# Performance work log

Measured on AMD Instinct MI355X. Metric: run time of the kernel, lower is better.

The kernel has to match this reference:

```python
import jax, jax.numpy as jnp
import numpy as np

D = 1024
H = 16
HD = D // H
EPS = 1e-9


def setup_inputs() -> dict:
    key = jax.random.key(0)
    ks = jax.random.split(key, 16)
    B, Lq, Lk = 8, 512, 1024
    s = 0.02
    return {
        "q": jax.random.normal(ks[0], (B, Lq, D), jnp.float32),
        "q_mask": jnp.ones((B, Lq), jnp.bool_),
        "kv": jax.random.normal(ks[1], (B, Lk, D), jnp.float32),
        "kv_mask": jnp.ones((B, Lk), jnp.bool_),
        # MultiheadAttention packed in-proj + out-proj
        "in_proj_w": jax.random.normal(ks[2], (3 * D, D), jnp.float32) * s,
        "in_proj_b": jnp.zeros((3 * D,), jnp.float32),
        "out_w": jax.random.normal(ks[3], (D, D), jnp.float32) * s,
        "out_b": jnp.zeros((D,), jnp.float32),
        # shared LayerNorm
        "ln_g": jnp.ones((D,), jnp.float32),
        "ln_b": jnp.zeros((D,), jnp.float32),
        # FFN
        "w1": jax.random.normal(ks[4], (4 * D, D), jnp.float32) * s,
        "b1": jnp.zeros((4 * D,), jnp.float32),
        "w2": jax.random.normal(ks[5], (D, 4 * D), jnp.float32) * s,
        "b2": jnp.zeros((D,), jnp.float32),
        # gate MLP
        "gw1": jax.random.normal(ks[6], (D, 2 * D), jnp.float32) * s,
        "gb1": jnp.zeros((D,), jnp.float32),
        "gw2": jax.random.normal(ks[7], (1, D), jnp.float32) * s,
        "gb2": jnp.zeros((1,), jnp.float32),
    }


def _layer_norm(x, g, b, eps=1e-5):
    mu = x.mean(-1, keepdims=True)
    var = ((x - mu) ** 2).mean(-1, keepdims=True)
    return (x - mu) * jax.lax.rsqrt(var + eps) * g + b


def reference(q, q_mask, kv, kv_mask, in_proj_w, in_proj_b, out_w, out_b,
              ln_g, ln_b, w1, b1, w2, b2, gw1, gb1, gw2, gb2):
    B, Lq, _ = q.shape
    Lk = kv.shape[1]
    # packed projections (torch Linear convention: x @ W.T + b)
    qp = (q @ in_proj_w[:D].T + in_proj_b[:D]).reshape(B, Lq, H, HD)
    kp = (kv @ in_proj_w[D:2 * D].T + in_proj_b[D:2 * D]).reshape(B, Lk, H, HD)
    vp = (kv @ in_proj_w[2 * D:].T + in_proj_b[2 * D:]).reshape(B, Lk, H, HD)
    scores = jnp.einsum('bqhd,bkhd->bhqk', qp, kp) / np.sqrt(HD)  # (B,H,Lq,Lk)
    scores = jnp.where(kv_mask[:, None, None, :], scores, -1e30)
    attn = jax.nn.softmax(scores, axis=-1)
    ctx = jnp.einsum('bhqk,bkhd->bqhd', attn, vp).reshape(B, Lq, D)
    attn_out = ctx @ out_w.T + out_b
    # entropy over keys, normalized by log(Lk), averaged over heads
    p = jnp.clip(attn, EPS)
    ent = -(p * jnp.log(p)).sum(-1) / jnp.log(jnp.float32(Lk))  # (B,H,Lq)
    ent = ent.mean(axis=1)[..., None]  # (B,Lq,1)
    conf = jnp.clip(1.0 - ent, 0.0, 1.0)
    # gate MLP on [q, attn_out]
    h = jax.nn.gelu(jnp.concatenate([q, attn_out], -1) @ gw1.T + gb1, approximate=False)
    g = jax.nn.sigmoid(h @ gw2.T + gb2) * conf
    q2 = _layer_norm(q + attn_out * g, ln_g, ln_b)
    ffn = jax.nn.gelu(q2 @ w1.T + b1, approximate=False) @ w2.T + b2
    q2 = _layer_norm(q2 + ffn, ln_g, ln_b)
    return q2, ent
```

## Files before the change

kernel.cpp:

```cpp
#include <hip/hip_runtime.h>
#include <cstdint>
#include <cstddef>

typedef __bf16 bf16;
typedef __bf16 bf16x8 __attribute__((ext_vector_type(8)));
typedef __bf16 bf16x4 __attribute__((ext_vector_type(4)));
typedef float  f32x4  __attribute__((ext_vector_type(4)));

#define GLOAD_LDS16(g, l) __builtin_amdgcn_global_load_lds( \
    (const __attribute__((address_space(1))) unsigned int*)(g), \
    (__attribute__((address_space(3))) unsigned int*)(l), 16, 0, 0)

static constexpr int D_  = 1024;
static constexpr int H_  = 16;
static constexpr int HD_ = 64;
static constexpr int B_  = 8;
static constexpr int LQ_ = 512;
static constexpr int LK_ = 1024;
static constexpr int MQ_ = B_ * LQ_;
static constexpr int MK_ = B_ * LK_;
static constexpr float LOG2E_ = 1.4426950408889634f;
static constexpr float INV_LN_LK_ = 0.14426950408889634f;
static constexpr float CSHIFT_ = 8.0f;

__device__ __forceinline__ float gelu_f(float v) {
    float v2 = v * v;
    float u = fmaf(0.035677408136f, v2, 0.7978845608028654f);
    float s = exp2f(v * u * -2.8853900817779268f);
    return v / (1.0f + s);
}

__global__ __launch_bounds__(256)
void cast_all_k(const float* __restrict__ ipw, const float* __restrict__ outw,
                const float* __restrict__ w1,  const float* __restrict__ w2,
                const float* __restrict__ gw1, const float* __restrict__ q,
                const float* __restrict__ kv,
                bf16* __restrict__ ipw_b, bf16* __restrict__ outw_b,
                bf16* __restrict__ w1_b,  bf16* __restrict__ w2_b,
                bf16* __restrict__ gw1_b, bf16* __restrict__ x_b,
                bf16* __restrict__ kv_b) {
    const int b = blockIdx.x, t = threadIdx.x;
    const float* src; bf16* dst; long e;
    if (b < 1536)       { src = ipw;  dst = ipw_b;  e = (long)b * 2048; }
    else if (b < 2048)  { src = outw; dst = outw_b; e = (long)(b - 1536) * 2048; }
    else if (b < 4096)  { src = w1;   dst = w1_b;   e = (long)(b - 2048) * 2048; }
    else if (b < 6144)  { src = w2;   dst = w2_b;   e = (long)(b - 4096) * 2048; }
    else if (b < 7168)  { src = gw1;  dst = gw1_b;  e = (long)(b - 6144) * 2048; }
    else if (b < 11264) { src = kv;   dst = kv_b;   e = (long)(b - 7168) * 2048; }
    else {
        long e2 = (long)(b - 11264) * 2048 + t * 8;
        float4 a = *(const float4*)(q + e2);
        float4 c = *(const float4*)(q + e2 + 4);
        bf16x8 o;
        o[0]=(bf16)a.x; o[1]=(bf16)a.y; o[2]=(bf16)a.z; o[3]=(bf16)a.w;
        o[4]=(bf16)c.x; o[5]=(bf16)c.y; o[6]=(bf16)c.z; o[7]=(bf16)c.w;
        long row = e2 >> 10, col = e2 & 1023;
        *(bf16x8*)(x_b + row * 2048 + col) = o;
        return;
    }
    e += t * 8;
    float4 a = *(const float4*)(src + e);
    float4 c = *(const float4*)(src + e + 4);
    bf16x8 o;
    o[0]=(bf16)a.x; o[1]=(bf16)a.y; o[2]=(bf16)a.z; o[3]=(bf16)a.w;
    o[4]=(bf16)c.x; o[5]=(bf16)c.y; o[6]=(bf16)c.z; o[7]=(bf16)c.w;
    *(bf16x8*)(dst + e) = o;
}

template<int SPLITK>
__device__ __forceinline__
void gemmP_body(const bf16* __restrict__ A, int lda,
                const bf16* __restrict__ W, int ldw,
                const float* __restrict__ bias,
                bf16* __restrict__ Cb0, bf16* __restrict__ Cb1, int ldcb,
                int K, int aoff, int woff) {
    __shared__ __attribute__((aligned(16))) bf16 LDSp[3 * 8192];
    const int gx = gridDim.x, gy = gridDim.y;
    const int nwg = gx * gy * gridDim.z;
    const int flat = blockIdx.x + gx * (blockIdx.y + gy * blockIdx.z);
    const int swz = (flat & 7) * (nwg >> 3) + (flat >> 3);
    int rem = swz, z = 0;
    if (SPLITK) { z = swz / (gx * gy); rem = swz - z * (gx * gy); }
    const int by = rem / gx, bx = rem - by * gx;
    if (SPLITK) { A += (size_t)z * aoff; W += (size_t)z * woff; }
    bf16* Cb = (SPLITK && z) ? Cb1 : Cb0;

    const int t = threadIdx.x;
    const int w = t >> 6, l = t & 63, l15 = l & 15, lg = l >> 4;
    const int row0 = by * 128, col0 = bx * 128;
    const int wr = (w >> 1) * 64, wc = (w & 1) * 64;

    const int sr = t >> 2;
    const int sc = ((t & 3) ^ ((sr >> 1) & 3)) << 3;
    const bf16* pA0 = A + (size_t)(row0 + sr) * lda + sc;
    const bf16* pA1 = A + (size_t)(row0 + 64 + sr) * lda + sc;
    const bf16* pW0 = W + (size_t)(col0 + sr) * ldw + sc;
    const bf16* pW1 = W + (size_t)(col0 + 64 + sr) * ldw + sc;
    const int lo0 = w * 512, lo1 = 2048 + w * 512;

    auto STAGE = [&](int kt, int slot) {
        bf16* base = (bf16*)LDSp + slot * 8192;
        const int kc = kt * 32;
        GLOAD_LDS16(pA0 + kc, base + lo0);
        GLOAD_LDS16(pA1 + kc, base + lo1);
        GLOAD_LDS16(pW0 + kc, base + 4096 + lo0);
        GLOAD_LDS16(pW1 + kc, base + 4096 + lo1);
    };

    f32x4 acc[4][4];
#pragma unroll
    for (int m = 0; m < 4; ++m)
#pragma unroll
        for (int n = 0; n < 4; ++n) acc[m][n] = f32x4{0.f, 0.f, 0.f, 0.f};

    const int nk = K >> 5;
    STAGE(0, 0); STAGE(1, 1);
    asm volatile("s_waitcnt vmcnt(4)" ::: "memory");
    __builtin_amdgcn_s_barrier();

    int s0 = 0, s1 = 1, s2 = 2;
    const int kcol = (lg ^ ((l15 >> 1) & 3)) << 3;
    for (int kt = 0; kt < nk; ++kt) {
        const bf16* bufA = (const bf16*)LDSp + s0 * 8192;
        const bf16* bufB = bufA + 4096;
        bf16x8 af[4], bf4[4];
#pragma unroll
        for (int m = 0; m < 4; ++m)
            af[m] = *(const bf16x8*)&bufA[(wr + m * 16 + l15) * 32 + kcol];
#pragma unroll
        for (int n = 0; n < 4; ++n)
            bf4[n] = *(const bf16x8*)&bufB[(wc + n * 16 + l15) * 32 + kcol];
        if (kt + 2 < nk) STAGE(kt + 2, s2);
        __builtin_amdgcn_s_setprio(1);
#pragma unroll
        for (int m = 0; m < 4; ++m)
#pragma unroll
            for (int n = 0; n < 4; ++n)
                acc[m][n] = __builtin_amdgcn_mfma_f32_16x16x32_bf16(af[m], bf4[n], acc[m][n], 0, 0, 0);
        __builtin_amdgcn_s_setprio(0);
        asm volatile("s_waitcnt lgkmcnt(0)" ::: "memory");
        __builtin_amdgcn_sched_barrier(0);
        if (kt + 2 < nk) {
            asm volatile("s_waitcnt vmcnt(4)" ::: "memory");
        } else {
            asm volatile("s_waitcnt vmcnt(0)" ::: "memory");
        }
        __builtin_amdgcn_s_barrier();
        const int tmp = s0; s0 = s1; s1 = s2; s2 = tmp;
    }

    float bvn[4];
#pragma unroll
    for (int n = 0; n < 4; ++n) bvn[n] = bias ? bias[col0 + wc + n * 16 + l15] : 0.f;
    const int erow = l >> 2, ec = (l & 3) * 16;
#pragma unroll
    for (int m = 0; m < 4; ++m) {
        bf16* ep = (bf16*)LDSp + ((m & 1) * 4 + w) * 1152;
#pragma unroll
        for (int n = 0; n < 4; ++n)
#pragma unroll
            for (int r = 0; r < 4; ++r)
                ep[(lg * 4 + r) * 72 + n * 16 + l15] = (bf16)(acc[m][n][r] + bvn[n]);
        asm volatile("s_waitcnt lgkmcnt(0)" ::: "memory");
        __builtin_amdgcn_sched_barrier(0);
        bf16x8 v8a = *(const bf16x8*)&ep[erow * 72 + ec];
        bf16x8 v8b = *(const bf16x8*)&ep[erow * 72 + ec + 8];
        const int grow = row0 + wr + m * 16 + erow;
        bf16* dst = Cb + (size_t)grow * ldcb + col0 + wc + ec;
        *(bf16x8*)dst = v8a;
        *(bf16x8*)(dst + 8) = v8b;
    }
}

__global__ __launch_bounds__(256, 2)
void gemmP_outproj_k(const bf16* A, const bf16* W, const float* bias, bf16* Cb) {
    gemmP_body<0>(A, 1024, W, 1024, bias, Cb, nullptr, 2048, 1024, 0, 0);
}
__global__ __launch_bounds__(256, 2)
void gemmP_gate2_k(const bf16* A, const bf16* W, bf16* C0, bf16* C1) {
    gemmP_body<1>(A, 2048, W, 2048, nullptr, C0, C1, 1024, 1024, 1024, 1024);
}
__global__ __launch_bounds__(256, 2)
void gemmP_ffn2_k(const bf16* A, const bf16* W, bf16* C0, bf16* C1) {
    gemmP_body<1>(A, 4096, W, 4096, nullptr, C0, C1, 1024, 2048, 2048, 2048);
}

template<int ACT, int ROWBIAS>
__device__ __forceinline__
void gemm128x256_body(bf16* LDSb, int by, int bx,
                      const bf16* __restrict__ A, int lda,
                      const bf16* __restrict__ W, int ldw,
                      const float* __restrict__ bias,
                      bf16* __restrict__ Cb, int ldcb, int K) {
    const int t = threadIdx.x;
    const int w = t >> 6, l = t & 63, l15 = l & 15, lg = l >> 4;
    const int wrr = w >> 2, wc = w & 3;
    const int row0 = by * 128, col0 = bx * 256;

    const int trow = t >> 2;
    const int scol = ((t & 3) ^ ((trow >> 1) & 3)) << 3;
    const bf16* pA  = A + (size_t)(row0 + trow) * lda + scol;
    const bf16* pB0 = W + (size_t)(col0 + trow) * ldw + scol;
    const bf16* pB1 = W + (size_t)(col0 + 128 + trow) * ldw + scol;
    const int ldsoA  = w * 512;
    const int ldsoB0 = 4096 + w * 512;
    const int ldsoB1 = 8192 + w * 512;

    f32x4 acc[4][4];
#pragma unroll
    for (int m = 0; m < 4; ++m)
#pragma unroll
        for (int n = 0; n < 4; ++n) acc[m][n] = f32x4{0.f, 0.f, 0.f, 0.f};

    const int nk = K >> 5;
    GLOAD_LDS16(pA,  LDSb + ldsoA);
    GLOAD_LDS16(pB0, LDSb + ldsoB0);
    GLOAD_LDS16(pB1, LDSb + ldsoB1);

    for (int kt = 0; kt < nk; ++kt) {
        const int cur = kt & 1;
        if (kt + 1 < nk) {
            const int kc = (kt + 1) * 32;
            bf16* d = LDSb + (cur ^ 1) * 12288;
            GLOAD_LDS16(pA + kc,  d + ldsoA);
            GLOAD_LDS16(pB0 + kc, d + ldsoB0);
            GLOAD_LDS16(pB1 + kc, d + ldsoB1);
            asm volatile("s_waitcnt vmcnt(3)" ::: "memory");
        } else {
            asm volatile("s_waitcnt vmcnt(0)" ::: "memory");
        }
        __builtin_amdgcn_s_barrier();
        const bf16* bufA = LDSb + cur * 12288;
        const bf16* bufB = bufA + 4096;
        const int kcol = (lg ^ ((l15 >> 1) & 3)) << 3;
        bf16x8 bf4[4];
#pragma unroll
        for (int n = 0; n < 4; ++n)
            bf4[n] = *(const bf16x8*)&bufB[(wc * 64 + n * 16 + l15) * 32 + kcol];
#pragma unroll
        for (int m = 0; m < 4; ++m) {
            bf16x8 afm = *(const bf16x8*)&bufA[(wrr * 64 + m * 16 + l15) * 32 + kcol];
#pragma unroll
            for (int n = 0; n < 4; ++n)
                acc[m][n] = __builtin_amdgcn_mfma_f32_16x16x32_bf16(afm, bf4[n], acc[m][n], 0, 0, 0);
        }
        asm volatile("s_waitcnt lgkmcnt(0)" ::: "memory");
        __builtin_amdgcn_sched_barrier(0);
        __builtin_amdgcn_s_barrier();
    }

    const int erow = l >> 2, ec = (l & 3) * 16;
    float bvn[4];
    if (!ROWBIAS) {
#pragma unroll
        for (int n = 0; n < 4; ++n) bvn[n] = bias[col0 + wc * 64 + n * 16 + l15];
    }
#pragma unroll
    for (int m = 0; m < 4; ++m) {
        float bvr[4];
        if (ROWBIAS) {
#pragma unroll
            for (int r = 0; r < 4; ++r)
                bvr[r] = bias[row0 + wrr * 64 + m * 16 + lg * 4 + r];
        }
        bf16* ep = LDSb + ((m & 1) * 8 + w) * 1152;
#pragma unroll
        for (int n = 0; n < 4; ++n)
#pragma unroll
            for (int r = 0; r < 4; ++r) {
                float v = acc[m][n][r] + (ROWBIAS ? bvr[r] : bvn[n]);
                if (ACT) v = gelu_f(v);
                ep[(lg * 4 + r) * 72 + n * 16 + l15] = (bf16)v;
            }
        asm volatile("s_waitcnt lgkmcnt(0)" ::: "memory");
        __builtin_amdgcn_sched_barrier(0);
        bf16x8 v8a = *(const bf16x8*)&ep[erow * 72 + ec];
        bf16x8 v8b = *(const bf16x8*)&ep[erow * 72 + ec + 8];
        const int grow = row0 + wrr * 64 + m * 16 + erow;
        bf16* dst = Cb + (size_t)grow * ldcb + col0 + wc * 64 + ec;
        *(bf16x8*)dst = v8a;
        *(bf16x8*)(dst + 8) = v8b;
    }
}

__global__ __launch_bounds__(512, 4)
void gemm_proj3_k(const bf16* __restrict__ xb, const bf16* __restrict__ kvb,
                  const bf16* __restrict__ ipw_b, const float* __restrict__ ipb,
                  bf16* __restrict__ Qp, bf16* __restrict__ Kp, bf16* __restrict__ Vt) {
    __shared__ __attribute__((aligned(16))) bf16 LDSb[2 * 12288];
    const int fb = blockIdx.x;
    if (fb < 256) {
        const int id = fb;
        const int swz = (id & 7) * 32 + (id >> 3);
        gemm128x256_body<0, 0>(LDSb, swz >> 2, swz & 3, kvb, 1024, ipw_b + 1024 * 1024, 1024,
                               ipb + 1024, Kp, 1024, 1024);
    } else if (fb < 512) {
        const int id = fb - 256;
        const int bx = (id & 7) * 4 + ((id >> 3) & 3);
        const int by = id >> 5;
        gemm128x256_body<0, 1>(LDSb, by, bx, ipw_b + 2048 * 1024, 1024, kvb, 1024,
                               ipb + 2048, Vt, 8192, 1024);
    } else {
        const int id = fb - 512;
        const int swz = (id & 7) * 16 + (id >> 3);
        gemm128x256_body<0, 0>(LDSb, swz >> 2, swz & 3, xb, 2048, ipw_b, 1024, ipb, Qp, 1024, 1024);
    }
}

__global__ __launch_bounds__(512, 4)
void gemmA_ffn1_k(const bf16* A, const bf16* W, const float* bias, bf16* Cb) {
    __shared__ __attribute__((aligned(16))) bf16 LDSb[2 * 12288];
    const int f = blockIdx.x + gridDim.x * blockIdx.y;
    const int x = f & 7, i = f >> 3;
    const int by = (x >> 1) * 8 + (i >> 3);
    const int bx = (x & 1) * 8 + (i & 7);
    gemm128x256_body<1, 0>(LDSb, by, bx, A, 1024, W, 1024, bias, Cb, 4096, 1024);
}

__device__ __forceinline__ float red16sum(float v) {
    v += __shfl_xor(v, 1, 64);
    v += __shfl_xor(v, 2, 64);
    v += __shfl_xor(v, 4, 64);
    v += __shfl_xor(v, 8, 64);
    return v;
}

__global__ __launch_bounds__(256)
void attn_k(const bf16* __restrict__ Qp, const bf16* __restrict__ Kp,
            const bf16* __restrict__ Vt, bf16* __restrict__ ctx,
            float* __restrict__ entm) {
    __shared__ __attribute__((aligned(16))) bf16 Ks[64 * 64];
    __shared__ __attribute__((aligned(16))) bf16 Vs[64 * 64];
    __shared__ __attribute__((aligned(16))) bf16 Ps[4][16 * 72];
    const int t = threadIdx.x, w = t >> 6, l = t & 63;
    const int l15 = l & 15, lg = l >> 4;
    const int h = blockIdx.x, b = blockIdx.y, qt = blockIdx.z;
    const int qrow0 = b * LQ_ + qt * 64 + w * 16;

    bf16x8 aq[2];
#pragma unroll
    for (int kk = 0; kk < 2; ++kk)
        aq[kk] = *(const bf16x8*)(Qp + (size_t)(qrow0 + l15) * D_ + h * HD_ + kk * 32 + lg * 8);

    const int r0 = t >> 3, r1 = 32 + (t >> 3), j = t & 7;
    const bf16* pK0 = Kp + (size_t)(b * LK_ + r0) * 1024 + h * HD_ + ((j ^ (r0 & 7)) << 3);
    const bf16* pK1 = Kp + (size_t)(b * LK_ + r1) * 1024 + h * HD_ + ((j ^ (r1 & 7)) << 3);
    const bf16* pV0 = Vt + (size_t)(h * HD_ + r0) * (size_t)MK_ + b * LK_ + ((j ^ (r0 & 7)) << 3);
    const bf16* pV1 = Vt + (size_t)(h * HD_ + r1) * (size_t)MK_ + b * LK_ + ((j ^ (r1 & 7)) << 3);
    const int ldsoL = w * 512, ldsoH = 2048 + w * 512;

    auto STAGE = [&](int c) {
        const size_t kadv = (size_t)c * 64 * 1024;
        const size_t vadv = (size_t)c * 64;
        GLOAD_LDS16(pK0 + kadv, (bf16*)Ks + ldsoL);
        GLOAD_LDS16(pK1 + kadv, (bf16*)Ks + ldsoH);
        GLOAD_LDS16(pV0 + vadv, (bf16*)Vs + ldsoL);
        GLOAD_LDS16(pV1 + vadv, (bf16*)Vs + ldsoH);
    };

    f32x4 o[4];
    float Zp[4], S1p[4];
#pragma unroll
    for (int n = 0; n < 4; ++n) o[n] = f32x4{0.f, 0.f, 0.f, 0.f};
#pragma unroll
    for (int r = 0; r < 4; ++r) { Zp[r] = 0.f; S1p[r] = 0.f; }

    const float K1 = 0.125f * LOG2E_;
    const float K0 = -CSHIFT_ * LOG2E_;
    const int swk = l15 & 7;

    for (int c = 0; c < LK_ / 64; ++c) {
        STAGE(c);
        asm volatile("s_waitcnt vmcnt(0)" ::: "memory");
        __builtin_amdgcn_s_barrier();

        f32x4 s[4];
#pragma unroll
        for (int n = 0; n < 4; ++n) {
            s[n] = f32x4{0.f, 0.f, 0.f, 0.f};
#pragma unroll
            for (int kk = 0; kk < 2; ++kk) {
                bf16x8 bk = *(const bf16x8*)&Ks[(n * 16 + l15) * 64 + ((((kk << 2) | lg) ^ swk) << 3)];
                s[n] = __builtin_amdgcn_mfma_f32_16x16x32_bf16(aq[kk], bk, s[n], 0, 0, 0);
            }
        }

        float p[4][4];
#pragma unroll
        for (int r = 0; r < 4; ++r) {
#pragma unroll
            for (int n = 0; n < 4; ++n) {
                float sv = s[n][r];
                float pv = exp2f(fmaf(sv, K1, K0));
                p[n][r] = pv;
                Zp[r] += pv;
                S1p[r] = fmaf(pv, sv, S1p[r]);
            }
        }

#pragma unroll
        for (int r = 0; r < 4; ++r)
#pragma unroll
            for (int n = 0; n < 4; ++n)
                Ps[w][(lg * 4 + r) * 72 + ((n ^ lg) << 4) + l15] = (bf16)p[n][r];

        bf16x8 ap[2];
#pragma unroll
        for (int kk = 0; kk < 2; ++kk)
            ap[kk] = *(const bf16x8*)&Ps[w][l15 * 72 + ((kk * 32 + lg * 8) ^ (((l15 >> 2) & 3) << 4))];
#pragma unroll
        for (int n = 0; n < 4; ++n)
#pragma unroll
            for (int kk = 0; kk < 2; ++kk) {
                bf16x8 bv = *(const bf16x8*)&Vs[(n * 16 + l15) * 64 + ((((kk << 2) | lg) ^ swk) << 3)];
                o[n] = __builtin_amdgcn_mfma_f32_16x16x32_bf16(ap[kk], bv, o[n], 0, 0, 0);
            }

        asm volatile("s_waitcnt lgkmcnt(0)" ::: "memory");
        __builtin_amdgcn_sched_barrier(0);
        __builtin_amdgcn_s_barrier();
    }

#pragma unroll
    for (int r = 0; r < 4; ++r) {
        float Zr = red16sum(Zp[r]);
        float S1r = red16sum(S1p[r]) * 0.125f;
        float inv = 1.0f / Zr;
        int grow = qrow0 + lg * 4 + r;
#pragma unroll
        for (int n = 0; n < 4; ++n)
            ctx[(size_t)grow * D_ + h * HD_ + n * 16 + l15] = (bf16)(o[n][r] * inv);
        if (l15 == 0) {
            float ent = (CSHIFT_ + logf(Zr) - S1r * inv) * INV_LN_LK_ * (1.0f / 16.0f);
            atomicAdd(&entm[grow], ent);
        }
    }
}

__device__ __forceinline__ float blk_sum(float v, float* sb) {
#pragma unroll
    for (int m = 1; m < 64; m <<= 1) v += __shfl_xor(v, m, 64);
    int w = threadIdx.x >> 6;
    __syncthreads();
    if ((threadIdx.x & 63) == 0) sb[w] = v;
    __syncthreads();
    return sb[0] + sb[1] + sb[2] + sb[3];
}
__device__ __forceinline__ float2 blk_sum2(float2 v, float* sb) {
#pragma unroll
    for (int m = 1; m < 64; m <<= 1) {
        v.x += __shfl_xor(v.x, m, 64);
        v.y += __shfl_xor(v.y, m, 64);
    }
    int w = threadIdx.x >> 6;
    __syncthreads();
    if ((threadIdx.x & 63) == 0) { sb[w * 2] = v.x; sb[w * 2 + 1] = v.y; }
    __syncthreads();
    return make_float2(sb[0] + sb[2] + sb[4] + sb[6], sb[1] + sb[3] + sb[5] + sb[7]);
}

__global__ __launch_bounds__(256)
void gate_ln1_k(const float* __restrict__ qin, const bf16* __restrict__ xb,
                const bf16* __restrict__ gp0, const bf16* __restrict__ gp1,
                const float* __restrict__ gb1, const float* __restrict__ gw2,
                const float* __restrict__ gb2, const float* __restrict__ entm,
                const float* __restrict__ lng, const float* __restrict__ lnb,
                bf16* __restrict__ q2b) {
    __shared__ float sb[8];
    const int row = blockIdx.x, t = threadIdx.x, c0 = t * 4;
    bf16x4 pa = *(const bf16x4*)(gp0 + (size_t)row * D_ + c0);
    bf16x4 pb = *(const bf16x4*)(gp1 + (size_t)row * D_ + c0);
    float4 hb = *(const float4*)(gb1 + c0);
    float h0 = gelu_f((float)pa[0] + (float)pb[0] + hb.x);
    float h1 = gelu_f((float)pa[1] + (float)pb[1] + hb.y);
    float h2 = gelu_f((float)pa[2] + (float)pb[2] + hb.z);
    float h3 = gelu_f((float)pa[3] + (float)pb[3] + hb.w);
    float4 g4 = *(const float4*)(gw2 + c0);
    float dot = h0 * g4.x + h1 * g4.y + h2 * g4.z + h3 * g4.w;
    dot = blk_sum(dot, sb);
    float g = 1.0f / (1.0f + expf(-(dot + gb2[0])));
    float conf = fminf(fmaxf(1.0f - entm[row], 0.0f), 1.0f);
    g *= conf;
    float4 qv = *(const float4*)(qin + (size_t)row * D_ + c0);
    bf16x4 a4 = *(const bf16x4*)(xb + (size_t)row * 2048 + 1024 + c0);
    float y[4] = { qv.x + (float)a4[0] * g, qv.y + (float)a4[1] * g,
                   qv.z + (float)a4[2] * g, qv.w + (float)a4[3] * g };
    float2 ss = blk_sum2(make_float2(y[0] + y[1] + y[2] + y[3],
                                     y[0]*y[0] + y[1]*y[1] + y[2]*y[2] + y[3]*y[3]), sb);
    float mu = ss.x * (1.0f / D_);
    float var = ss.y * (1.0f / D_) - mu * mu;
    float rs = rsqrtf(var + 1e-5f);
    float4 gg = *(const float4*)(lng + c0);
    float4 bb = *(const float4*)(lnb + c0);
    bf16x4 ob;
    ob[0] = (bf16)((y[0] - mu) * rs * gg.x + bb.x);
    ob[1] = (bf16)((y[1] - mu) * rs * gg.y + bb.y);
    ob[2] = (bf16)((y[2] - mu) * rs * gg.z + bb.z);
    ob[3] = (bf16)((y[3] - mu) * rs * gg.w + bb.w);
    *(bf16x4*)(q2b + (size_t)row * D_ + c0) = ob;
}

__global__ __launch_bounds__(256)
void ln2_k(const bf16* __restrict__ q2b, const bf16* __restrict__ fp0,
           const bf16* __restrict__ fp1, const float* __restrict__ b2,
           const float* __restrict__ lng, const float* __restrict__ lnb,
           float* __restrict__ outp) {
    __shared__ float sb[8];
    const int row = blockIdx.x, t = threadIdx.x, c0 = t * 4;
    bf16x4 a4 = *(const bf16x4*)(q2b + (size_t)row * D_ + c0);
    bf16x4 f0 = *(const bf16x4*)(fp0 + (size_t)row * D_ + c0);
    bf16x4 f1 = *(const bf16x4*)(fp1 + (size_t)row * D_ + c0);
    float4 bv = *(const float4*)(b2 + c0);
    float y[4] = { (float)a4[0] + (float)f0[0] + (float)f1[0] + bv.x,
                   (float)a4[1] + (float)f0[1] + (float)f1[1] + bv.y,
                   (float)a4[2] + (float)f0[2] + (float)f1[2] + bv.z,
                   (float)a4[3] + (float)f0[3] + (float)f1[3] + bv.w };
    float2 ss = blk_sum2(make_float2(y[0] + y[1] + y[2] + y[3],
                                     y[0]*y[0] + y[1]*y[1] + y[2]*y[2] + y[3]*y[3]), sb);
    float mu = ss.x * (1.0f / D_);
    float var = ss.y * (1.0f / D_) - mu * mu;
    float rs = rsqrtf(var + 1e-5f);
    float4 gg = *(const float4*)(lng + c0);
    float4 bb = *(const float4*)(lnb + c0);
    *(float4*)(outp + (size_t)row * D_ + c0) = make_float4(
        (y[0] - mu) * rs * gg.x + bb.x, (y[1] - mu) * rs * gg.y + bb.y,
        (y[2] - mu) * rs * gg.z + bb.z, (y[3] - mu) * rs * gg.w + bb.w);
}

extern "C" void kernel_launch(void* const* d_in, const int* in_sizes, int n_in,
                              void* d_out, int out_size, void* d_ws, size_t ws_size,
                              hipStream_t stream) {
    (void)in_sizes; (void)n_in; (void)out_size; (void)ws_size;
    const float* q    = (const float*)d_in[0];
    const float* kv   = (const float*)d_in[2];
    const float* ipw  = (const float*)d_in[4];
    const float* ipb  = (const float*)d_in[5];
    const float* outw = (const float*)d_in[6];
    const float* outb = (const float*)d_in[7];
    const float* lng  = (const float*)d_in[8];
    const float* lnb  = (const float*)d_in[9];
    const float* w1   = (const float*)d_in[10];
    const float* b1   = (const float*)d_in[11];
    const float* w2   = (const float*)d_in[12];
    const float* b2   = (const float*)d_in[13];
    const float* gw1  = (const float*)d_in[14];
    const float* gb1  = (const float*)d_in[15];
    const float* gw2  = (const float*)d_in[16];
    const float* gb2  = (const float*)d_in[17];

    char* ws = (char*)d_ws;
    const size_t MB = 1u << 20;
    bf16*  ipw_b  = (bf16*)(ws + 0);
    bf16*  outw_b = (bf16*)(ws + 6 * MB);
    bf16*  w1_b   = (bf16*)(ws + 8 * MB);
    bf16*  w2_b   = (bf16*)(ws + 16 * MB);
    bf16*  gw1_b  = (bf16*)(ws + 24 * MB);
    bf16*  x_b    = (bf16*)(ws + 28 * MB);
    bf16*  kv_b   = (bf16*)(ws + 44 * MB);
    bf16*  Qp     = (bf16*)(ws + 60 * MB);
    bf16*  Kp     = (bf16*)(ws + 68 * MB);
    bf16*  Vt     = (bf16*)(ws + 84 * MB);
    bf16*  ctx    = (bf16*)(ws + 100 * MB);
    bf16*  gp0    = (bf16*)(ws + 44 * MB);
    bf16*  gp1    = (bf16*)(ws + 52 * MB);
    bf16*  q2b    = (bf16*)(ws + 100 * MB);
    bf16*  h1     = (bf16*)(ws + 44 * MB);
    bf16*  fp0    = (bf16*)(ws + 28 * MB);
    bf16*  fp1    = (bf16*)(ws + 0);

    float* out  = (float*)d_out;
    float* entm = out + (size_t)MQ_ * D_;

    (void)hipMemsetAsync(entm, 0, (size_t)MQ_ * sizeof(float), stream);

    cast_all_k<<<13312, 256, 0, stream>>>(ipw, outw, w1, w2, gw1, q, kv,
                                          ipw_b, outw_b, w1_b, w2_b, gw1_b, x_b, kv_b);

    gemm_proj3_k<<<640, 512, 0, stream>>>(x_b, kv_b, ipw_b, ipb, Qp, Kp, Vt);
    attn_k<<<dim3(H_, B_, LQ_ / 64), 256, 0, stream>>>(Qp, Kp, Vt, ctx, entm);
    gemmP_outproj_k<<<dim3(8, 32), 256, 0, stream>>>(ctx, outw_b, outb, x_b + 1024);
    gemmP_gate2_k<<<dim3(8, 32, 2), 256, 0, stream>>>(x_b, gw1_b, gp0, gp1);
    gate_ln1_k<<<MQ_, 256, 0, stream>>>(q, x_b, gp0, gp1, gb1, gw2, gb2, entm, lng, lnb, q2b);
    gemmA_ffn1_k<<<dim3(16, 32), 512, 0, stream>>>(q2b, w1_b, b1, h1);
    gemmP_ffn2_k<<<dim3(8, 32, 2), 256, 0, stream>>>(h1, w2_b, fp0, fp1);
    ln2_k<<<MQ_, 256, 0, stream>>>(q2b, fp0, fp1, b2, lng, lnb, out);
}
```

Measured before the change: 276.9 us.

## Restructure split-K GEMMs, merge out-proj with gate half, widen attention blocks

```diff
diff --git a/kernel.cpp b/kernel.cpp
--- a/kernel.cpp
+++ b/kernel.cpp
@@ -67,24 +67,12 @@
     *(bf16x8*)(dst + e) = o;
 }
 
-template<int SPLITK>
 __device__ __forceinline__
-void gemmP_body(const bf16* __restrict__ A, int lda,
+void gemmP_core(bf16* LDSp, int by, int bx,
+                const bf16* __restrict__ A, int lda,
                 const bf16* __restrict__ W, int ldw,
                 const float* __restrict__ bias,
-                bf16* __restrict__ Cb0, bf16* __restrict__ Cb1, int ldcb,
-                int K, int aoff, int woff) {
-    __shared__ __attribute__((aligned(16))) bf16 LDSp[3 * 8192];
-    const int gx = gridDim.x, gy = gridDim.y;
-    const int nwg = gx * gy * gridDim.z;
-    const int flat = blockIdx.x + gx * (blockIdx.y + gy * blockIdx.z);
-    const int swz = (flat & 7) * (nwg >> 3) + (flat >> 3);
-    int rem = swz, z = 0;
-    if (SPLITK) { z = swz / (gx * gy); rem = swz - z * (gx * gy); }
-    const int by = rem / gx, bx = rem - by * gx;
-    if (SPLITK) { A += (size_t)z * aoff; W += (size_t)z * woff; }
-    bf16* Cb = (SPLITK && z) ? Cb1 : Cb0;
-
+                bf16* __restrict__ Cb, int ldcb, int K) {
     const int t = threadIdx.x;
     const int w = t >> 6, l = t & 63, l15 = l & 15, lg = l >> 4;
     const int row0 = by * 128, col0 = bx * 128;
@@ -99,7 +87,7 @@
     const int lo0 = w * 512, lo1 = 2048 + w * 512;
 
     auto STAGE = [&](int kt, int slot) {
-        bf16* base = (bf16*)LDSp + slot * 8192;
+        bf16* base = LDSp + slot * 8192;
         const int kc = kt * 32;
         GLOAD_LDS16(pA0 + kc, base + lo0);
         GLOAD_LDS16(pA1 + kc, base + lo1);
@@ -121,7 +109,7 @@
     int s0 = 0, s1 = 1, s2 = 2;
     const int kcol = (lg ^ ((l15 >> 1) & 3)) << 3;
     for (int kt = 0; kt < nk; ++kt) {
-        const bf16* bufA = (const bf16*)LDSp + s0 * 8192;
+        const bf16* bufA = LDSp + s0 * 8192;
         const bf16* bufB = bufA + 4096;
         bf16x8 af[4], bf4[4];
 #pragma unroll
@@ -155,7 +143,7 @@
     const int erow = l >> 2, ec = (l & 3) * 16;
 #pragma unroll
     for (int m = 0; m < 4; ++m) {
-        bf16* ep = (bf16*)LDSp + ((m & 1) * 4 + w) * 1152;
+        bf16* ep = LDSp + ((m & 1) * 4 + w) * 1152;
 #pragma unroll
         for (int n = 0; n < 4; ++n)
 #pragma unroll
@@ -173,16 +161,42 @@
 }
 
 __global__ __launch_bounds__(256, 2)
-void gemmP_outproj_k(const bf16* A, const bf16* W, const float* bias, bf16* Cb) {
-    gemmP_body<0>(A, 1024, W, 1024, bias, Cb, nullptr, 2048, 1024, 0, 0);
-}
+void gemm_opq_k(const bf16* __restrict__ ctx, const bf16* __restrict__ outw_b,
+                const float* __restrict__ outb, const bf16* __restrict__ xb,
+                const bf16* __restrict__ gw1_b, bf16* __restrict__ ao_out,
+                bf16* __restrict__ gp0) {
+    __shared__ __attribute__((aligned(16))) bf16 LDSp[3 * 8192];
+    const int fb = blockIdx.x;
+    const int id = fb & 255;
+    const int swz = (id & 7) * 32 + (id >> 3);
+    const int by = swz >> 3, bx = swz & 7;
+    if (fb < 256)
+        gemmP_core(LDSp, by, bx, ctx, 1024, outw_b, 1024, outb, ao_out, 2048, 1024);
+    else
+        gemmP_core(LDSp, by, bx, xb, 2048, gw1_b, 2048, nullptr, gp0, 1024, 1024);
+}
+
 __global__ __launch_bounds__(256, 2)
-void gemmP_gate2_k(const bf16* A, const bf16* W, bf16* C0, bf16* C1) {
-    gemmP_body<1>(A, 2048, W, 2048, nullptr, C0, C1, 1024, 1024, 1024, 1024);
-}
+void gemm_gatek_k(const bf16* __restrict__ xb, const bf16* __restrict__ gw1_b,
+                  bf16* __restrict__ gp1) {
+    __shared__ __attribute__((aligned(16))) bf16 LDSp[3 * 8192];
+    const int id = blockIdx.x;
+    const int swz = (id & 7) * 32 + (id >> 3);
+    gemmP_core(LDSp, swz >> 3, swz & 7, xb + 1024, 2048, gw1_b + 1024, 2048,
+               nullptr, gp1, 1024, 1024);
+}
+
 __global__ __launch_bounds__(256, 2)
-void gemmP_ffn2_k(const bf16* A, const bf16* W, bf16* C0, bf16* C1) {
-    gemmP_body<1>(A, 4096, W, 4096, nullptr, C0, C1, 1024, 2048, 2048, 2048);
+void gemm_ffn2_k(const bf16* __restrict__ h1, const bf16* __restrict__ w2_b,
+                 bf16* __restrict__ f0, bf16* __restrict__ f1,
+                 bf16* __restrict__ f2, bf16* __restrict__ f3) {
+    __shared__ __attribute__((aligned(16))) bf16 LDSp[3 * 8192];
+    const int flat = blockIdx.x;
+    const int swz = (flat & 7) * 128 + (flat >> 3);
+    const int z = swz >> 8, rem = swz & 255;
+    bf16* Cb = (z == 0) ? f0 : (z == 1) ? f1 : (z == 2) ? f2 : f3;
+    gemmP_core(LDSp, rem >> 3, rem & 7, h1 + z * 1024, 4096, w2_b + z * 1024, 4096,
+               nullptr, Cb, 1024, 1024);
 }
 
 template<int ACT, int ROWBIAS>
@@ -325,37 +339,31 @@
     return v;
 }
 
-__global__ __launch_bounds__(256)
+__global__ __launch_bounds__(512)
 void attn_k(const bf16* __restrict__ Qp, const bf16* __restrict__ Kp,
             const bf16* __restrict__ Vt, bf16* __restrict__ ctx,
             float* __restrict__ entm) {
     __shared__ __attribute__((aligned(16))) bf16 Ks[64 * 64];
     __shared__ __attribute__((aligned(16))) bf16 Vs[64 * 64];
-    __shared__ __attribute__((aligned(16))) bf16 Ps[4][16 * 72];
+    __shared__ __attribute__((aligned(16))) bf16 Ps[8][16 * 72];
     const int t = threadIdx.x, w = t >> 6, l = t & 63;
     const int l15 = l & 15, lg = l >> 4;
     const int h = blockIdx.x, b = blockIdx.y, qt = blockIdx.z;
-    const int qrow0 = b * LQ_ + qt * 64 + w * 16;
+    const int qrow0 = b * LQ_ + qt * 128 + w * 16;
 
     bf16x8 aq[2];
 #pragma unroll
     for (int kk = 0; kk < 2; ++kk)
         aq[kk] = *(const bf16x8*)(Qp + (size_t)(qrow0 + l15) * D_ + h * HD_ + kk * 32 + lg * 8);
 
-    const int r0 = t >> 3, r1 = 32 + (t >> 3), j = t & 7;
-    const bf16* pK0 = Kp + (size_t)(b * LK_ + r0) * 1024 + h * HD_ + ((j ^ (r0 & 7)) << 3);
-    const bf16* pK1 = Kp + (size_t)(b * LK_ + r1) * 1024 + h * HD_ + ((j ^ (r1 & 7)) << 3);
-    const bf16* pV0 = Vt + (size_t)(h * HD_ + r0) * (size_t)MK_ + b * LK_ + ((j ^ (r0 & 7)) << 3);
-    const bf16* pV1 = Vt + (size_t)(h * HD_ + r1) * (size_t)MK_ + b * LK_ + ((j ^ (r1 & 7)) << 3);
-    const int ldsoL = w * 512, ldsoH = 2048 + w * 512;
+    const int r = t >> 3, j = t & 7;
+    const bf16* pK = Kp + (size_t)(b * LK_ + r) * 1024 + h * HD_ + ((j ^ (r & 7)) << 3);
+    const bf16* pV = Vt + (size_t)(h * HD_ + r) * (size_t)MK_ + b * LK_ + ((j ^ (r & 7)) << 3);
+    const int ldso = w * 512;
 
     auto STAGE = [&](int c) {
-        const size_t kadv = (size_t)c * 64 * 1024;
-        const size_t vadv = (size_t)c * 64;
-        GLOAD_LDS16(pK0 + kadv, (bf16*)Ks + ldsoL);
-        GLOAD_LDS16(pK1 + kadv, (bf16*)Ks + ldsoH);
-        GLOAD_LDS16(pV0 + vadv, (bf16*)Vs + ldsoL);
-        GLOAD_LDS16(pV1 + vadv, (bf16*)Vs + ldsoH);
+        GLOAD_LDS16(pK + (size_t)c * 64 * 1024, (bf16*)Ks + ldso);
+        GLOAD_LDS16(pV + (size_t)c * 64,        (bf16*)Vs + ldso);
     };
 
     f32x4 o[4];
@@ -363,7 +371,7 @@
 #pragma unroll
     for (int n = 0; n < 4; ++n) o[n] = f32x4{0.f, 0.f, 0.f, 0.f};
 #pragma unroll
-    for (int r = 0; r < 4; ++r) { Zp[r] = 0.f; S1p[r] = 0.f; }
+    for (int r2 = 0; r2 < 4; ++r2) { Zp[r2] = 0.f; S1p[r2] = 0.f; }
 
     const float K1 = 0.125f * LOG2E_;
     const float K0 = -CSHIFT_ * LOG2E_;
@@ -387,22 +395,22 @@
 
         float p[4][4];
 #pragma unroll
-        for (int r = 0; r < 4; ++r) {
+        for (int r2 = 0; r2 < 4; ++r2) {
 #pragma unroll
             for (int n = 0; n < 4; ++n) {
-                float sv = s[n][r];
+                float sv = s[n][r2];
                 float pv = exp2f(fmaf(sv, K1, K0));
-                p[n][r] = pv;
-                Zp[r] += pv;
-                S1p[r] = fmaf(pv, sv, S1p[r]);
+                p[n][r2] = pv;
+                Zp[r2] += pv;
+                S1p[r2] = fmaf(pv, sv, S1p[r2]);
             }
         }
 
 #pragma unroll
-        for (int r = 0; r < 4; ++r)
+        for (int r2 = 0; r2 < 4; ++r2)
 #pragma unroll
             for (int n = 0; n < 4; ++n)
-                Ps[w][(lg * 4 + r) * 72 + ((n ^ lg) << 4) + l15] = (bf16)p[n][r];
+                Ps[w][(lg * 4 + r2) * 72 + ((n ^ lg) << 4) + l15] = (bf16)p[n][r2];
 
         bf16x8 ap[2];
 #pragma unroll
@@ -422,14 +430,14 @@
     }
 
 #pragma unroll
-    for (int r = 0; r < 4; ++r) {
-        float Zr = red16sum(Zp[r]);
-        float S1r = red16sum(S1p[r]) * 0.125f;
+    for (int r2 = 0; r2 < 4; ++r2) {
+        float Zr = red16sum(Zp[r2]);
+        float S1r = red16sum(S1p[r2]) * 0.125f;
         float inv = 1.0f / Zr;
-        int grow = qrow0 + lg * 4 + r;
+        int grow = qrow0 + lg * 4 + r2;
 #pragma unroll
         for (int n = 0; n < 4; ++n)
-            ctx[(size_t)grow * D_ + h * HD_ + n * 16 + l15] = (bf16)(o[n][r] * inv);
+            ctx[(size_t)grow * D_ + h * HD_ + n * 16 + l15] = (bf16)(o[n][r2] * inv);
         if (l15 == 0) {
             float ent = (CSHIFT_ + logf(Zr) - S1r * inv) * INV_LN_LK_ * (1.0f / 16.0f);
             atomicAdd(&entm[grow], ent);
@@ -460,7 +468,7 @@
 }
 
 __global__ __launch_bounds__(256)
-void gate_ln1_k(const float* __restrict__ qin, const bf16* __restrict__ xb,
+void gate_ln1_k(const bf16* __restrict__ xb,
                 const bf16* __restrict__ gp0, const bf16* __restrict__ gp1,
                 const float* __restrict__ gb1, const float* __restrict__ gw2,
                 const float* __restrict__ gb2, const float* __restrict__ entm,
@@ -481,10 +489,10 @@
     float g = 1.0f / (1.0f + expf(-(dot + gb2[0])));
     float conf = fminf(fmaxf(1.0f - entm[row], 0.0f), 1.0f);
     g *= conf;
-    float4 qv = *(const float4*)(qin + (size_t)row * D_ + c0);
+    bf16x4 qv = *(const bf16x4*)(xb + (size_t)row * 2048 + c0);
     bf16x4 a4 = *(const bf16x4*)(xb + (size_t)row * 2048 + 1024 + c0);
-    float y[4] = { qv.x + (float)a4[0] * g, qv.y + (float)a4[1] * g,
-                   qv.z + (float)a4[2] * g, qv.w + (float)a4[3] * g };
+    float y[4] = { (float)qv[0] + (float)a4[0] * g, (float)qv[1] + (float)a4[1] * g,
+                   (float)qv[2] + (float)a4[2] * g, (float)qv[3] + (float)a4[3] * g };
     float2 ss = blk_sum2(make_float2(y[0] + y[1] + y[2] + y[3],
                                      y[0]*y[0] + y[1]*y[1] + y[2]*y[2] + y[3]*y[3]), sb);
     float mu = ss.x * (1.0f / D_);
@@ -501,20 +509,24 @@
 }
 
 __global__ __launch_bounds__(256)
-void ln2_k(const bf16* __restrict__ q2b, const bf16* __restrict__ fp0,
-           const bf16* __restrict__ fp1, const float* __restrict__ b2,
+void ln2_k(const bf16* __restrict__ q2b, const bf16* __restrict__ f0,
+           const bf16* __restrict__ f1, const bf16* __restrict__ f2,
+           const bf16* __restrict__ f3, const float* __restrict__ b2,
            const float* __restrict__ lng, const float* __restrict__ lnb,
            float* __restrict__ outp) {
     __shared__ float sb[8];
     const int row = blockIdx.x, t = threadIdx.x, c0 = t * 4;
     bf16x4 a4 = *(const bf16x4*)(q2b + (size_t)row * D_ + c0);
-    bf16x4 f0 = *(const bf16x4*)(fp0 + (size_t)row * D_ + c0);
-    bf16x4 f1 = *(const bf16x4*)(fp1 + (size_t)row * D_ + c0);
+    bf16x4 p0 = *(const bf16x4*)(f0 + (size_t)row * D_ + c0);
+    bf16x4 p1 = *(const bf16x4*)(f1 + (size_t)row * D_ + c0);
+    bf16x4 p2 = *(const bf16x4*)(f2 + (size_t)row * D_ + c0);
+    bf16x4 p3 = *(const bf16x4*)(f3 + (size_t)row * D_ + c0);
     float4 bv = *(const float4*)(b2 + c0);
-    float y[4] = { (float)a4[0] + (float)f0[0] + (float)f1[0] + bv.x,
-                   (float)a4[1] + (float)f0[1] + (float)f1[1] + bv.y,
-                   (float)a4[2] + (float)f0[2] + (float)f1[2] + bv.z,
-                   (float)a4[3] + (float)f0[3] + (float)f1[3] + bv.w };
+    float y[4];
+#pragma unroll
+    for (int i = 0; i < 4; ++i)
+        y[i] = (float)a4[i] + (float)p0[i] + (float)p1[i] + (float)p2[i] + (float)p3[i]
+             + ((const float*)&bv)[i];
     float2 ss = blk_sum2(make_float2(y[0] + y[1] + y[2] + y[3],
                                      y[0]*y[0] + y[1]*y[1] + y[2]*y[2] + y[3]*y[3]), sb);
     float mu = ss.x * (1.0f / D_);
@@ -566,7 +578,9 @@
     bf16*  q2b    = (bf16*)(ws + 100 * MB);
     bf16*  h1     = (bf16*)(ws + 44 * MB);
     bf16*  fp0    = (bf16*)(ws + 28 * MB);
-    bf16*  fp1    = (bf16*)(ws + 0);
+    bf16*  fp1    = (bf16*)(ws + 36 * MB);
+    bf16*  fp2    = (bf16*)(ws + 0);
+    bf16*  fp3    = (bf16*)(ws + 8 * MB);
 
     float* out  = (float*)d_out;
     float* entm = out + (size_t)MQ_ * D_;
@@ -577,11 +591,11 @@
                                           ipw_b, outw_b, w1_b, w2_b, gw1_b, x_b, kv_b);
 
     gemm_proj3_k<<<640, 512, 0, stream>>>(x_b, kv_b, ipw_b, ipb, Qp, Kp, Vt);
-    attn_k<<<dim3(H_, B_, LQ_ / 64), 256, 0, stream>>>(Qp, Kp, Vt, ctx, entm);
-    gemmP_outproj_k<<<dim3(8, 32), 256, 0, stream>>>(ctx, outw_b, outb, x_b + 1024);
-    gemmP_gate2_k<<<dim3(8, 32, 2), 256, 0, stream>>>(x_b, gw1_b, gp0, gp1);
-    gate_ln1_k<<<MQ_, 256, 0, stream>>>(q, x_b, gp0, gp1, gb1, gw2, gb2, entm, lng, lnb, q2b);
+    attn_k<<<dim3(H_, B_, LQ_ / 128), 512, 0, stream>>>(Qp, Kp, Vt, ctx, entm);
+    gemm_opq_k<<<512, 256, 0, stream>>>(ctx, outw_b, outb, x_b, gw1_b, x_b + 1024, gp0);
+    gemm_gatek_k<<<256, 256, 0, stream>>>(x_b, gw1_b, gp1);
+    gate_ln1_k<<<MQ_, 256, 0, stream>>>(x_b, gp0, gp1, gb1, gw2, gb2, entm, lng, lnb, q2b);
     gemmA_ffn1_k<<<dim3(16, 32), 512, 0, stream>>>(q2b, w1_b, b1, h1);
-    gemmP_ffn2_k<<<dim3(8, 32, 2), 256, 0, stream>>>(h1, w2_b, fp0, fp1);
-    ln2_k<<<MQ_, 256, 0, stream>>>(q2b, fp0, fp1, b2, lng, lnb, out);
-}
+    gemm_ffn2_k<<<1024, 256, 0, stream>>>(h1, w2_b, fp0, fp1, fp2, fp3);
+    ln2_k<<<MQ_, 256, 0, stream>>>(q2b, fp0, fp1, fp2, fp3, b2, lng, lnb, out);
+}
```

Result: no change. 275.9 us, median of 2 (-0.4%).
